# Performance work log

Hardware: AMD Instinct MI355X
Metric: run time of the kernel (lower is better)

Reference implementation:

```python
import jax, jax.numpy as jnp
import numpy as np

N, E, D, K = 32768, 16384, 4, 8          # nodes, hyperedges, edges/node, nodes/edge
IN_DIM, OUT_DIM, EDGE_DIM, NUM_HEADS = 128, 128, 64, 8


def setup_inputs() -> dict:
    key = jax.random.key(0)
    ks = jax.random.split(key, 16)
    s_in = 1.0 / np.sqrt(IN_DIM)
    s_out = 1.0 / np.sqrt(OUT_DIM)
    s_edge = 1.0 / np.sqrt(EDGE_DIM)
    return {
        "x": jax.random.normal(ks[0], (N, IN_DIM), jnp.float32),
        "edge_attr": jax.random.normal(ks[1], (E, EDGE_DIM), jnp.float32),
        "node_edges": jax.random.randint(ks[2], (N, D), 0, E),   # hyperedges containing each node
        "edge_nodes": jax.random.randint(ks[3], (E, K), 0, N),   # nodes inside each hyperedge
        "W_lin": jax.random.normal(ks[4], (OUT_DIM, IN_DIM), jnp.float32) * s_in,
        "W_edge": jax.random.normal(ks[5], (OUT_DIM, EDGE_DIM), jnp.float32) * s_edge,
        "Wq": jax.random.normal(ks[6], (OUT_DIM, OUT_DIM), jnp.float32) * s_out,
        "Wk": jax.random.normal(ks[7], (OUT_DIM, OUT_DIM), jnp.float32) * s_out,
        "Wv": jax.random.normal(ks[8], (OUT_DIM, OUT_DIM), jnp.float32) * s_out,
        "bq": jnp.zeros((OUT_DIM,), jnp.float32),
        "bk": jnp.zeros((OUT_DIM,), jnp.float32),
        "bv": jnp.zeros((OUT_DIM,), jnp.float32),
        "Wo": jax.random.normal(ks[9], (OUT_DIM, OUT_DIM), jnp.float32) * s_out,
        "bo": jnp.zeros((OUT_DIM,), jnp.float32),
    }


def reference(x, edge_attr, node_edges, edge_nodes,
              W_lin, W_edge, Wq, Wk, Wv, bq, bk, bv, Wo, bo):
    n, out_dim = x.shape[0], W_lin.shape[0]
    hd = out_dim // NUM_HEADS
    L = node_edges.shape[1] * edge_nodes.shape[1]  # D*K keys per node

    Wh = x @ W_lin.T                               # [N, out]
    We = edge_attr @ W_edge.T                      # [E, out]

    u_idx = edge_nodes[node_edges]                 # [N, D, K] neighbor node ids
    vals = Wh[u_idx]                               # [N, D, K, out]
    keys = vals + We[node_edges][:, :, None, :]    # key = Wh[u] + We[e]
    keys = keys.reshape(n, L, out_dim)
    vals = vals.reshape(n, L, out_dim)

    # torch nn.MultiheadAttention: single query per node (query = Wh[v])
    q = (Wh @ Wq.T + bq).reshape(n, NUM_HEADS, hd)
    k = (keys @ Wk.T + bk).reshape(n, L, NUM_HEADS, hd)
    v = (vals @ Wv.T + bv).reshape(n, L, NUM_HEADS, hd)

    scores = jnp.einsum('nhd,nlhd->nhl', q, k) / jnp.sqrt(jnp.asarray(hd, q.dtype))
    attn = jax.nn.softmax(scores, axis=-1)         # [N, H, L]
    ctx = jnp.einsum('nhl,nlhd->nhd', attn, v).reshape(n, out_dim)
    out = ctx @ Wo.T + bo
    return jax.nn.relu(out)
```

## Files before the change

kernel.cpp:

```cpp
#include <hip/hip_runtime.h>

#define N_NODES 32768
#define N_EDGES 16384
#define DEG 4
#define KPE 8
#define DIM 128
#define EDIM 64

typedef float f32x4 __attribute__((ext_vector_type(4)));
typedef __bf16 bf16x8 __attribute__((ext_vector_type(8)));
typedef __bf16 bf16x2 __attribute__((ext_vector_type(2)));
typedef unsigned short u16x8 __attribute__((ext_vector_type(8)));
typedef unsigned int u32;
typedef unsigned int u32x4 __attribute__((ext_vector_type(4)));
typedef int i32x4 __attribute__((ext_vector_type(4)));

static __device__ __forceinline__ unsigned short f2bf(float f) {
  union { float f; unsigned int u; } v; v.f = f;
  unsigned int r = (v.u + 0x7FFFu + ((v.u >> 16) & 1u)) >> 16;
  return (unsigned short)r;
}
static __device__ __forceinline__ float bflo(unsigned int v) {
  union { unsigned int u; float f; } x; x.u = v << 16; return x.f;
}
static __device__ __forceinline__ float bfhi(unsigned int v) {
  union { unsigned int u; float f; } x; x.u = v & 0xffff0000u; return x.f;
}

#if __has_builtin(__builtin_amdgcn_fdot2_f32_bf16)
static __device__ __forceinline__ float dot2bf(unsigned int a, unsigned int b, float c) {
  return __builtin_amdgcn_fdot2_f32_bf16(
      __builtin_bit_cast(bf16x2, a), __builtin_bit_cast(bf16x2, b), c, false);
}
#else
static __device__ __forceinline__ float dot2bf(unsigned int a, unsigned int b, float c) {
  c = fmaf(bflo(a), bflo(b), c);
  return fmaf(bfhi(a), bfhi(b), c);
}
#endif

__global__ __launch_bounds__(256) void wprep_kernel(
    const float* __restrict__ Wq, const float* __restrict__ Wk,
    const float* __restrict__ Wv, const float* __restrict__ Wlin,
    const float* __restrict__ Wedge, const float* __restrict__ Wo,
    const int* __restrict__ node_edges, const int* __restrict__ enodes,
    unsigned short* __restrict__ CW, unsigned short* __restrict__ CWE,
    unsigned short* __restrict__ Wob, int* __restrict__ uidx)
{
  int id = blockIdx.x * 256 + threadIdx.x;
  if (id < 384 * 128) {
    int j = id >> 7, i = id & 127;
    const float* wrow; float scale = 1.0f;
    if (j < 128)      { wrow = Wq + j * 128; scale = 0.25f; }
    else if (j < 256) { wrow = Wk + (j - 128) * 128; }
    else              { wrow = Wv + (j - 256) * 128; }
    float s = 0.f;
    #pragma unroll 8
    for (int m = 0; m < 128; ++m) s += wrow[m] * Wlin[m * 128 + i];
    CW[id] = f2bf(s * scale);
  } else if (id < 384 * 128 + 128 * 64) {
    int id2 = id - 384 * 128; int j = id2 >> 6, t = id2 & 63;
    float s = 0.f;
    #pragma unroll 8
    for (int m = 0; m < 128; ++m) s += Wk[j * 128 + m] * Wedge[m * 64 + t];
    CWE[id2] = f2bf(s);
  } else if (id < 384 * 128 + 128 * 64 + 128 * 128) {
    int id3 = id - (384 * 128 + 128 * 64);
    Wob[id3] = f2bf(Wo[id3]);
  } else {
    int t = id - (384 * 128 + 128 * 64 + 128 * 128);
    int e = node_edges[t];
    i32x4 a = *(const i32x4*)(enodes + (size_t)e * KPE);
    i32x4 b = *(const i32x4*)(enodes + (size_t)e * KPE + 4);
    *(i32x4*)(uidx + (size_t)t * KPE)     = a;
    *(i32x4*)(uidx + (size_t)t * KPE + 4) = b;
  }
}

__global__ __launch_bounds__(256) void g12_kernel(
    const float* __restrict__ x, const unsigned short* __restrict__ CW,
    const float* __restrict__ bq, const float* __restrict__ bv,
    unsigned short* __restrict__ qb, unsigned short* __restrict__ Kb,
    unsigned short* __restrict__ Vb,
    const float* __restrict__ ea, const unsigned short* __restrict__ CWE,
    const float* __restrict__ bk, unsigned short* __restrict__ WeKb)
{
  const int wave = threadIdx.x >> 6, lane = threadIdx.x & 63;
  const int r16 = lane & 15, quad = lane >> 4;

  if (blockIdx.x < 512) {
    const int m0 = blockIdx.x * 64 + wave * 16;
    u16x8 av[4];
    const float* arow = x + (size_t)(m0 + r16) * DIM + quad * 8;
    #pragma unroll
    for (int kk = 0; kk < 4; ++kk) {
      float4 a0 = *(const float4*)(arow + kk * 32);
      float4 a1 = *(const float4*)(arow + kk * 32 + 4);
      u16x8 au;
      au[0] = f2bf(a0.x); au[1] = f2bf(a0.y); au[2] = f2bf(a0.z); au[3] = f2bf(a0.w);
      au[4] = f2bf(a1.x); au[5] = f2bf(a1.y); au[6] = f2bf(a1.z); au[7] = f2bf(a1.w);
      av[kk] = au;
    }
    #pragma unroll
    for (int g = 0; g < 6; ++g) {
      f32x4 acc[4];
      const f32x4 z = {0.f, 0.f, 0.f, 0.f};
      acc[0] = z; acc[1] = z; acc[2] = z; acc[3] = z;
      #pragma unroll
      for (int kk = 0; kk < 4; ++kk) {
        #pragma unroll
        for (int s = 0; s < 4; ++s) {
          u16x8 bu = *(const u16x8*)(CW + (size_t)(g * 64 + s * 16 + r16) * DIM + kk * 32 + quad * 8);
          acc[s] = __builtin_amdgcn_mfma_f32_16x16x32_bf16(
              __builtin_bit_cast(bf16x8, av[kk]), __builtin_bit_cast(bf16x8, bu), acc[s], 0, 0, 0);
        }
      }
      const int arr = g >> 1;
      const int colbase = (g & 1) * 64;
      unsigned short* dst = arr == 0 ? qb : (arr == 1 ? Kb : Vb);
      #pragma unroll
      for (int s = 0; s < 4; ++s) {
        int j = colbase + s * 16 + r16;
        float bias = arr == 0 ? 0.25f * bq[j] : (arr == 2 ? bv[j] : 0.f);
        #pragma unroll
        for (int r = 0; r < 4; ++r) {
          int m = m0 + quad * 4 + r;
          dst[(size_t)m * DIM + j] = f2bf(acc[s][r] + bias);
        }
      }
    }
  } else {
    const int idx = blockIdx.x - 512;
    const int m0 = (idx >> 1) * 64 + wave * 16;
    const int n0 = (idx & 1) * 64;
    f32x4 acc[4];
    const f32x4 z = {0.f, 0.f, 0.f, 0.f};
    acc[0] = z; acc[1] = z; acc[2] = z; acc[3] = z;
    const float* arow = ea + (size_t)(m0 + r16) * EDIM + quad * 8;
    #pragma unroll
    for (int kk = 0; kk < 2; ++kk) {
      float4 a0 = *(const float4*)(arow + kk * 32);
      float4 a1 = *(const float4*)(arow + kk * 32 + 4);
      u16x8 au;
      au[0] = f2bf(a0.x); au[1] = f2bf(a0.y); au[2] = f2bf(a0.z); au[3] = f2bf(a0.w);
      au[4] = f2bf(a1.x); au[5] = f2bf(a1.y); au[6] = f2bf(a1.z); au[7] = f2bf(a1.w);
      bf16x8 av = __builtin_bit_cast(bf16x8, au);
      #pragma unroll
      for (int s = 0; s < 4; ++s) {
        u16x8 bu = *(const u16x8*)(CWE + (size_t)(n0 + s * 16 + r16) * EDIM + kk * 32 + quad * 8);
        acc[s] = __builtin_amdgcn_mfma_f32_16x16x32_bf16(
            av, __builtin_bit_cast(bf16x8, bu), acc[s], 0, 0, 0);
      }
    }
    #pragma unroll
    for (int s = 0; s < 4; ++s) {
      int j = n0 + s * 16 + r16;
      float bias = bk[j];
      #pragma unroll
      for (int r = 0; r < 4; ++r) {
        int m = m0 + quad * 4 + r;
        WeKb[(size_t)m * DIM + j] = f2bf(acc[s][r] + bias);
      }
    }
  }
}

__global__ __launch_bounds__(256) void g2b_kernel(
    const unsigned short* __restrict__ Kb, const unsigned short* __restrict__ WeKb,
    const int* __restrict__ enodes, unsigned short* __restrict__ Ke)
{
  const int wave = threadIdx.x >> 6, lane = threadIdx.x & 63;
  const int e = blockIdx.x * 4 + wave;

  const int* ep = enodes + (size_t)e * KPE;
  i32x4 a = *(const i32x4*)ep;
  i32x4 b = *(const i32x4*)(ep + 4);
  u32 we = ((const u32*)(WeKb + (size_t)e * DIM))[lane];

  int id[8] = {a.x, a.y, a.z, a.w, b.x, b.y, b.z, b.w};
  u32 kr[8];
  #pragma unroll
  for (int t = 0; t < 8; ++t)
    kr[t] = ((const u32*)(Kb + (size_t)id[t] * DIM))[lane];

  const float wl = bflo(we), wh = bfhi(we);
  u32* out = (u32*)(Ke + (size_t)e * KPE * DIM);
  #pragma unroll
  for (int t = 0; t < 8; ++t) {
    u32 pk = (u32)f2bf(bflo(kr[t]) + wl) | ((u32)f2bf(bfhi(kr[t]) + wh) << 16);
    out[t * (DIM / 2) + lane] = pk;
  }
}

__global__ __launch_bounds__(64, 3) void attn_kernel(
    const unsigned short* __restrict__ qb, const unsigned short* __restrict__ Ke,
    const unsigned short* __restrict__ Vb,
    const int* __restrict__ nedges, const int* __restrict__ uidx,
    unsigned short* __restrict__ ctxb)
{
  __shared__ __align__(16) float ldsP[8][36];
  const int lane = threadIdx.x;
  const int n = blockIdx.x;
  const int l = lane & 31, half = lane >> 5;
  const int h = lane >> 3;
  const int c0 = lane * 2;

  i32x4 e4 = __builtin_nontemporal_load((const i32x4*)(nedges + (size_t)n * DEG));
  const i32x4* up = (const i32x4*)(uidx + (size_t)n * 32);
  i32x4 m0 = __builtin_nontemporal_load(up + 0);
  i32x4 m1 = __builtin_nontemporal_load(up + 1);
  i32x4 m2 = __builtin_nontemporal_load(up + 2);
  i32x4 m3 = __builtin_nontemporal_load(up + 3);
  i32x4 m4 = __builtin_nontemporal_load(up + 4);
  i32x4 m5 = __builtin_nontemporal_load(up + 5);
  i32x4 m6 = __builtin_nontemporal_load(up + 6);
  i32x4 m7 = __builtin_nontemporal_load(up + 7);

  const u32x4* qp = (const u32x4*)(qb + (size_t)n * DIM + half * 64);
  u32x4 qv[8];
  #pragma unroll
  for (int ch = 0; ch < 8; ++ch) qv[ch] = __builtin_nontemporal_load(qp + ch);

  asm volatile("" ::: "memory");

  const int d = l >> 3, kk = l & 7;
  int el = d == 0 ? e4.x : (d == 1 ? e4.y : (d == 2 ? e4.z : e4.w));
  const unsigned short* krow = Ke + ((size_t)el * KPE + kk) * DIM + half * 64;
  u32x4 kc[8];
  #pragma unroll
  for (int ch = 0; ch < 8; ++ch) kc[ch] = *(const u32x4*)(krow + ch * 8);

  asm volatile("" ::: "memory");

  u32 vv[32];
#define VLOAD(t, row) vv[t] = *(const u32*)(Vb + (size_t)(row) * DIM + c0)
  VLOAD(0,  m0.x); VLOAD(1,  m0.y); VLOAD(2,  m0.z); VLOAD(3,  m0.w);
  VLOAD(4,  m1.x); VLOAD(5,  m1.y); VLOAD(6,  m1.z); VLOAD(7,  m1.w);
  VLOAD(8,  m2.x); VLOAD(9,  m2.y); VLOAD(10, m2.z); VLOAD(11, m2.w);
  VLOAD(12, m3.x); VLOAD(13, m3.y); VLOAD(14, m3.z); VLOAD(15, m3.w);
  VLOAD(16, m4.x); VLOAD(17, m4.y); VLOAD(18, m4.z); VLOAD(19, m4.w);
  VLOAD(20, m5.x); VLOAD(21, m5.y); VLOAD(22, m5.z); VLOAD(23, m5.w);
  VLOAD(24, m6.x); VLOAD(25, m6.y); VLOAD(26, m6.z); VLOAD(27, m6.w);
  VLOAD(28, m7.x); VLOAD(29, m7.y); VLOAD(30, m7.z); VLOAD(31, m7.w);
#undef VLOAD

  asm volatile("" ::: "memory");

  float s[4] = {0.f, 0.f, 0.f, 0.f};
  #pragma unroll
  for (int ch = 0; ch < 8; ++ch) {
    const int hi = ch >> 1;
    float t = s[hi];
    t = dot2bf(qv[ch].x, kc[ch].x, t);
    t = dot2bf(qv[ch].y, kc[ch].y, t);
    t = dot2bf(qv[ch].z, kc[ch].z, t);
    t = dot2bf(qv[ch].w, kc[ch].w, t);
    s[hi] = t;
  }

  #pragma unroll
  for (int hi = 0; hi < 4; ++hi) {
    float vmax = s[hi];
    #pragma unroll
    for (int off = 16; off >= 1; off >>= 1)
      vmax = fmaxf(vmax, __shfl_xor(vmax, off, 32));
    float ex = __expf(s[hi] - vmax);
    float sum = ex;
    #pragma unroll
    for (int off = 16; off >= 1; off >>= 1)
      sum += __shfl_xor(sum, off, 32);
    ldsP[half * 4 + hi][l] = ex / sum;
  }

  float a0 = 0.f, a1 = 0.f;
  #pragma unroll
  for (int t = 0; t < 8; ++t) {
    float4 p4 = *(const float4*)&ldsP[h][t * 4];
    a0 = fmaf(p4.x, bflo(vv[t * 4 + 0]), a0); a1 = fmaf(p4.x, bfhi(vv[t * 4 + 0]), a1);
    a0 = fmaf(p4.y, bflo(vv[t * 4 + 1]), a0); a1 = fmaf(p4.y, bfhi(vv[t * 4 + 1]), a1);
    a0 = fmaf(p4.z, bflo(vv[t * 4 + 2]), a0); a1 = fmaf(p4.z, bfhi(vv[t * 4 + 2]), a1);
    a0 = fmaf(p4.w, bflo(vv[t * 4 + 3]), a0); a1 = fmaf(p4.w, bfhi(vv[t * 4 + 3]), a1);
  }
  unsigned int pk = (unsigned int)f2bf(a0) | ((unsigned int)f2bf(a1) << 16);
  __builtin_nontemporal_store(pk, (u32*)(ctxb + (size_t)n * DIM + c0));
}

__global__ __launch_bounds__(256) void g4_kernel(
    const unsigned short* __restrict__ ctxb, const unsigned short* __restrict__ Wob,
    const float* __restrict__ bo, float* __restrict__ out)
{
  const int wave = threadIdx.x >> 6, lane = threadIdx.x & 63;
  const int r16 = lane & 15, quad = lane >> 4;
  const int m0 = blockIdx.x * 64 + wave * 16;
  const int n0 = blockIdx.y * 64;

  f32x4 acc[4];
  const f32x4 z = {0.f, 0.f, 0.f, 0.f};
  acc[0] = z; acc[1] = z; acc[2] = z; acc[3] = z;

  #pragma unroll
  for (int kk = 0; kk < 4; ++kk) {
    u16x8 au = *(const u16x8*)(ctxb + (size_t)(m0 + r16) * DIM + kk * 32 + quad * 8);
    bf16x8 av = __builtin_bit_cast(bf16x8, au);
    #pragma unroll
    for (int s = 0; s < 4; ++s) {
      u16x8 bu = *(const u16x8*)(Wob + (size_t)(n0 + s * 16 + r16) * DIM + kk * 32 + quad * 8);
      acc[s] = __builtin_amdgcn_mfma_f32_16x16x32_bf16(
          av, __builtin_bit_cast(bf16x8, bu), acc[s], 0, 0, 0);
    }
  }

  #pragma unroll
  for (int s = 0; s < 4; ++s) {
    int j = n0 + s * 16 + r16;
    float bias = bo[j];
    #pragma unroll
    for (int r = 0; r < 4; ++r) {
      int m = m0 + quad * 4 + r;
      float v = acc[s][r] + bias;
      out[(size_t)m * DIM + j] = v > 0.f ? v : 0.f;
    }
  }
}

extern "C" void kernel_launch(void* const* d_in, const int* in_sizes, int n_in,
                              void* d_out, int out_size, void* d_ws, size_t ws_size,
                              hipStream_t stream)
{
  const float* x     = (const float*)d_in[0];
  const float* ea    = (const float*)d_in[1];
  const int* nedges  = (const int*)d_in[2];
  const int* enodes  = (const int*)d_in[3];
  const float* Wlin  = (const float*)d_in[4];
  const float* Wedge = (const float*)d_in[5];
  const float* Wq    = (const float*)d_in[6];
  const float* Wk    = (const float*)d_in[7];
  const float* Wv    = (const float*)d_in[8];
  const float* bq    = (const float*)d_in[9];
  const float* bk    = (const float*)d_in[10];
  const float* bv    = (const float*)d_in[11];
  const float* Wo    = (const float*)d_in[12];
  const float* bo    = (const float*)d_in[13];
  float* out = (float*)d_out;

  unsigned short* wsp = (unsigned short*)d_ws;
  unsigned short* CW   = wsp;  wsp += 384 * 128;
  unsigned short* CWE  = wsp;  wsp += 128 * 64;
  unsigned short* Wob  = wsp;  wsp += 128 * 128;
  unsigned short* qb   = wsp;  wsp += (size_t)N_NODES * DIM;
  unsigned short* Kb   = wsp;  wsp += (size_t)N_NODES * DIM;
  unsigned short* Vb   = wsp;  wsp += (size_t)N_NODES * DIM;
  unsigned short* WeKb = wsp;  wsp += (size_t)N_EDGES * DIM;
  unsigned short* ctxb = wsp;  wsp += (size_t)N_NODES * DIM;
  int* uidx = (int*)wsp;       wsp += (size_t)N_NODES * 32 * 2;
  unsigned short* Ke   = wsp;  wsp += (size_t)N_EDGES * KPE * DIM;

  wprep_kernel<<<dim3(800), dim3(256), 0, stream>>>(
      Wq, Wk, Wv, Wlin, Wedge, Wo, nedges, enodes, CW, CWE, Wob, uidx);
  g12_kernel<<<dim3(1024), dim3(256), 0, stream>>>(x, CW, bq, bv, qb, Kb, Vb, ea, CWE, bk, WeKb);
  g2b_kernel<<<dim3(N_EDGES / 4), dim3(256), 0, stream>>>(Kb, WeKb, enodes, Ke);
  attn_kernel<<<dim3(32768), dim3(64), 0, stream>>>(qb, Ke, Vb, nedges, uidx, ctxb);
  g4_kernel<<<dim3(512, 2), dim3(256), 0, stream>>>(ctxb, Wob, bo, out);
}
```

Before: 219.6 us.

## Restructure attention edge-centric with reverse index and per-edge score and context kernels

```diff
diff --git a/kernel.cpp b/kernel.cpp
--- a/kernel.cpp
+++ b/kernel.cpp
@@ -6,6 +6,7 @@
 #define KPE 8
 #define DIM 128
 #define EDIM 64
+#define MAXC 64
 
 typedef float f32x4 __attribute__((ext_vector_type(4)));
 typedef __bf16 bf16x8 __attribute__((ext_vector_type(8)));
@@ -26,6 +27,12 @@
 static __device__ __forceinline__ float bfhi(unsigned int v) {
   union { unsigned int u; float f; } x; x.u = v & 0xffff0000u; return x.f;
 }
+static __device__ __forceinline__ float f16tof(unsigned short h) {
+  return (float)__builtin_bit_cast(_Float16, h);
+}
+static __device__ __forceinline__ unsigned short ftof16(float f) {
+  return __builtin_bit_cast(unsigned short, (_Float16)f);
+}
 
 #if __has_builtin(__builtin_amdgcn_fdot2_f32_bf16)
 static __device__ __forceinline__ float dot2bf(unsigned int a, unsigned int b, float c) {
@@ -39,13 +46,18 @@
 }
 #endif
 
+__global__ __launch_bounds__(256) void zcnt_kernel(int* __restrict__ cnt)
+{
+  cnt[blockIdx.x * 256 + threadIdx.x] = 0;
+}
+
 __global__ __launch_bounds__(256) void wprep_kernel(
     const float* __restrict__ Wq, const float* __restrict__ Wk,
     const float* __restrict__ Wv, const float* __restrict__ Wlin,
     const float* __restrict__ Wedge, const float* __restrict__ Wo,
-    const int* __restrict__ node_edges, const int* __restrict__ enodes,
+    const int* __restrict__ node_edges,
     unsigned short* __restrict__ CW, unsigned short* __restrict__ CWE,
-    unsigned short* __restrict__ Wob, int* __restrict__ uidx)
+    unsigned short* __restrict__ Wob, int* __restrict__ cnt, int* __restrict__ rev)
 {
   int id = blockIdx.x * 256 + threadIdx.x;
   if (id < 384 * 128) {
@@ -69,11 +81,11 @@
     Wob[id3] = f2bf(Wo[id3]);
   } else {
     int t = id - (384 * 128 + 128 * 64 + 128 * 128);
-    int e = node_edges[t];
-    i32x4 a = *(const i32x4*)(enodes + (size_t)e * KPE);
-    i32x4 b = *(const i32x4*)(enodes + (size_t)e * KPE + 4);
-    *(i32x4*)(uidx + (size_t)t * KPE)     = a;
-    *(i32x4*)(uidx + (size_t)t * KPE + 4) = b;
+    if (t < N_NODES * DEG) {
+      int e = node_edges[t];
+      int pos = atomicAdd(&cnt[e], 1);
+      if (pos < MAXC) rev[(size_t)e * MAXC + pos] = t;
+    }
   }
 }
 
@@ -165,160 +177,178 @@
   }
 }
 
-__global__ __launch_bounds__(256) void g2b_kernel(
-    const unsigned short* __restrict__ Kb, const unsigned short* __restrict__ WeKb,
-    const int* __restrict__ enodes, unsigned short* __restrict__ Ke)
+__global__ __launch_bounds__(256) void escore_kernel(
+    const unsigned short* __restrict__ qb, const unsigned short* __restrict__ Kb,
+    const unsigned short* __restrict__ WeKb, const int* __restrict__ enodes,
+    const int* __restrict__ cnt, const int* __restrict__ rev,
+    unsigned short* __restrict__ S)
 {
   const int wave = threadIdx.x >> 6, lane = threadIdx.x & 63;
   const int e = blockIdx.x * 4 + wave;
-
-  const int* ep = enodes + (size_t)e * KPE;
-  i32x4 a = *(const i32x4*)ep;
-  i32x4 b = *(const i32x4*)(ep + 4);
-  u32 we = ((const u32*)(WeKb + (size_t)e * DIM))[lane];
-
-  int id[8] = {a.x, a.y, a.z, a.w, b.x, b.y, b.z, b.w};
-  u32 kr[8];
-  #pragma unroll
-  for (int t = 0; t < 8; ++t)
-    kr[t] = ((const u32*)(Kb + (size_t)id[t] * DIM))[lane];
-
-  const float wl = bflo(we), wh = bfhi(we);
-  u32* out = (u32*)(Ke + (size_t)e * KPE * DIM);
-  #pragma unroll
-  for (int t = 0; t < 8; ++t) {
-    u32 pk = (u32)f2bf(bflo(kr[t]) + wl) | ((u32)f2bf(bfhi(kr[t]) + wh) << 16);
-    out[t * (DIM / 2) + lane] = pk;
-  }
-}
-
-__global__ __launch_bounds__(64, 3) void attn_kernel(
-    const unsigned short* __restrict__ qb, const unsigned short* __restrict__ Ke,
-    const unsigned short* __restrict__ Vb,
-    const int* __restrict__ nedges, const int* __restrict__ uidx,
-    unsigned short* __restrict__ ctxb)
-{
-  __shared__ __align__(16) float ldsP[8][36];
-  const int lane = threadIdx.x;
-  const int n = blockIdx.x;
-  const int l = lane & 31, half = lane >> 5;
-  const int h = lane >> 3;
-  const int c0 = lane * 2;
-
-  i32x4 e4 = __builtin_nontemporal_load((const i32x4*)(nedges + (size_t)n * DEG));
-  const i32x4* up = (const i32x4*)(uidx + (size_t)n * 32);
-  i32x4 m0 = __builtin_nontemporal_load(up + 0);
-  i32x4 m1 = __builtin_nontemporal_load(up + 1);
-  i32x4 m2 = __builtin_nontemporal_load(up + 2);
-  i32x4 m3 = __builtin_nontemporal_load(up + 3);
-  i32x4 m4 = __builtin_nontemporal_load(up + 4);
-  i32x4 m5 = __builtin_nontemporal_load(up + 5);
-  i32x4 m6 = __builtin_nontemporal_load(up + 6);
-  i32x4 m7 = __builtin_nontemporal_load(up + 7);
-
-  const u32x4* qp = (const u32x4*)(qb + (size_t)n * DIM + half * 64);
-  u32x4 qv[8];
-  #pragma unroll
-  for (int ch = 0; ch < 8; ++ch) qv[ch] = __builtin_nontemporal_load(qp + ch);
-
-  asm volatile("" ::: "memory");
-
-  const int d = l >> 3, kk = l & 7;
-  int el = d == 0 ? e4.x : (d == 1 ? e4.y : (d == 2 ? e4.z : e4.w));
-  const unsigned short* krow = Ke + ((size_t)el * KPE + kk) * DIM + half * 64;
-  u32x4 kc[8];
-  #pragma unroll
-  for (int ch = 0; ch < 8; ++ch) kc[ch] = *(const u32x4*)(krow + ch * 8);
-
-  asm volatile("" ::: "memory");
-
-  u32 vv[32];
-#define VLOAD(t, row) vv[t] = *(const u32*)(Vb + (size_t)(row) * DIM + c0)
-  VLOAD(0,  m0.x); VLOAD(1,  m0.y); VLOAD(2,  m0.z); VLOAD(3,  m0.w);
-  VLOAD(4,  m1.x); VLOAD(5,  m1.y); VLOAD(6,  m1.z); VLOAD(7,  m1.w);
-  VLOAD(8,  m2.x); VLOAD(9,  m2.y); VLOAD(10, m2.z); VLOAD(11, m2.w);
-  VLOAD(12, m3.x); VLOAD(13, m3.y); VLOAD(14, m3.z); VLOAD(15, m3.w);
-  VLOAD(16, m4.x); VLOAD(17, m4.y); VLOAD(18, m4.z); VLOAD(19, m4.w);
-  VLOAD(20, m5.x); VLOAD(21, m5.y); VLOAD(22, m5.z); VLOAD(23, m5.w);
-  VLOAD(24, m6.x); VLOAD(25, m6.y); VLOAD(26, m6.z); VLOAD(27, m6.w);
-  VLOAD(28, m7.x); VLOAD(29, m7.y); VLOAD(30, m7.z); VLOAD(31, m7.w);
-#undef VLOAD
-
-  asm volatile("" ::: "memory");
-
-  float s[4] = {0.f, 0.f, 0.f, 0.f};
-  #pragma unroll
-  for (int ch = 0; ch < 8; ++ch) {
-    const int hi = ch >> 1;
-    float t = s[hi];
-    t = dot2bf(qv[ch].x, kc[ch].x, t);
-    t = dot2bf(qv[ch].y, kc[ch].y, t);
-    t = dot2bf(qv[ch].z, kc[ch].z, t);
-    t = dot2bf(qv[ch].w, kc[ch].w, t);
-    s[hi] = t;
-  }
-
+  const int g = lane >> 3, j = lane & 7;
+
+  int c_n = cnt[e]; if (c_n > MAXC) c_n = MAXC;
+  if (c_n == 0) return;
+  int rv = rev[(size_t)e * MAXC + lane];
+
+  int mid = enodes[(size_t)e * KPE + g];
+  u32x4 k0 = *(const u32x4*)(Kb + (size_t)mid * DIM + j * 16);
+  u32x4 k1 = *(const u32x4*)(Kb + (size_t)mid * DIM + j * 16 + 8);
+  u32x4 w0 = *(const u32x4*)(WeKb + (size_t)e * DIM + j * 16);
+  u32x4 w1 = *(const u32x4*)(WeKb + (size_t)e * DIM + j * 16 + 8);
+
+  int pk = __shfl(rv, 0);
+  u32x4 qa0 = *(const u32x4*)(qb + (size_t)(pk >> 2) * DIM + j * 16);
+  u32x4 qa1 = *(const u32x4*)(qb + (size_t)(pk >> 2) * DIM + j * 16 + 8);
+
+  for (int c = 0; c < c_n; ++c) {
+    const int n = pk >> 2, d = pk & 3;
+    u32x4 q0 = qa0, q1 = qa1;
+    if (c + 1 < c_n) {
+      pk = __shfl(rv, c + 1);
+      qa0 = *(const u32x4*)(qb + (size_t)(pk >> 2) * DIM + j * 16);
+      qa1 = *(const u32x4*)(qb + (size_t)(pk >> 2) * DIM + j * 16 + 8);
+    }
+    float s = 0.f;
+    s = dot2bf(q0.x, k0.x, s); s = dot2bf(q0.y, k0.y, s);
+    s = dot2bf(q0.z, k0.z, s); s = dot2bf(q0.w, k0.w, s);
+    s = dot2bf(q1.x, k1.x, s); s = dot2bf(q1.y, k1.y, s);
+    s = dot2bf(q1.z, k1.z, s); s = dot2bf(q1.w, k1.w, s);
+    s = dot2bf(q0.x, w0.x, s); s = dot2bf(q0.y, w0.y, s);
+    s = dot2bf(q0.z, w0.z, s); s = dot2bf(q0.w, w0.w, s);
+    s = dot2bf(q1.x, w1.x, s); s = dot2bf(q1.y, w1.y, s);
+    s = dot2bf(q1.z, w1.z, s); s = dot2bf(q1.w, w1.w, s);
+    S[(size_t)n * 256 + d * 64 + g * 8 + j] = ftof16(s);
+  }
+}
+
+__global__ __launch_bounds__(256) void nsm_kernel(unsigned short* __restrict__ SP)
+{
+  const int wave = threadIdx.x >> 6, lane = threadIdx.x & 63;
+  const int n = blockIdx.x * 4 + wave;
+  const int l = lane & 31, hp = lane >> 5;
+  unsigned short* row = SP + (size_t)n * 256;
+
+  uint2 sv = *(const uint2*)(row + l * 8 + hp * 4);
+  float s4[4] = { f16tof(sv.x & 0xffff), f16tof(sv.x >> 16),
+                  f16tof(sv.y & 0xffff), f16tof(sv.y >> 16) };
+  unsigned short pr[4];
   #pragma unroll
   for (int hi = 0; hi < 4; ++hi) {
-    float vmax = s[hi];
+    float vmax = s4[hi];
     #pragma unroll
     for (int off = 16; off >= 1; off >>= 1)
       vmax = fmaxf(vmax, __shfl_xor(vmax, off, 32));
-    float ex = __expf(s[hi] - vmax);
+    float ex = __expf(s4[hi] - vmax);
     float sum = ex;
     #pragma unroll
     for (int off = 16; off >= 1; off >>= 1)
       sum += __shfl_xor(sum, off, 32);
-    ldsP[half * 4 + hi][l] = ex / sum;
-  }
-
-  float a0 = 0.f, a1 = 0.f;
-  #pragma unroll
-  for (int t = 0; t < 8; ++t) {
-    float4 p4 = *(const float4*)&ldsP[h][t * 4];
-    a0 = fmaf(p4.x, bflo(vv[t * 4 + 0]), a0); a1 = fmaf(p4.x, bfhi(vv[t * 4 + 0]), a1);
-    a0 = fmaf(p4.y, bflo(vv[t * 4 + 1]), a0); a1 = fmaf(p4.y, bfhi(vv[t * 4 + 1]), a1);
-    a0 = fmaf(p4.z, bflo(vv[t * 4 + 2]), a0); a1 = fmaf(p4.z, bfhi(vv[t * 4 + 2]), a1);
-    a0 = fmaf(p4.w, bflo(vv[t * 4 + 3]), a0); a1 = fmaf(p4.w, bfhi(vv[t * 4 + 3]), a1);
-  }
-  unsigned int pk = (unsigned int)f2bf(a0) | ((unsigned int)f2bf(a1) << 16);
-  __builtin_nontemporal_store(pk, (u32*)(ctxb + (size_t)n * DIM + c0));
+    pr[hi] = ftof16(ex / sum);
+  }
+  #pragma unroll
+  for (int hi = 0; hi < 4; ++hi)
+    row[(hp * 4 + hi) * 32 + l] = pr[hi];
+}
+
+__global__ __launch_bounds__(256) void ectx_kernel(
+    const unsigned short* __restrict__ Vb, const unsigned short* __restrict__ P,
+    const int* __restrict__ enodes, const int* __restrict__ cnt,
+    const int* __restrict__ rev, unsigned short* __restrict__ ctxp)
+{
+  const int wave = threadIdx.x >> 6, lane = threadIdx.x & 63;
+  const int e = blockIdx.x * 4 + wave;
+  const int c0 = lane * 2, h = lane >> 3;
+
+  int c_n = cnt[e]; if (c_n > MAXC) c_n = MAXC;
+  if (c_n == 0) return;
+  int rv = rev[(size_t)e * MAXC + lane];
+
+  const int* ep = enodes + (size_t)e * KPE;
+  i32x4 a4 = *(const i32x4*)ep;
+  i32x4 b4 = *(const i32x4*)(ep + 4);
+  int id[8] = {a4.x, a4.y, a4.z, a4.w, b4.x, b4.y, b4.z, b4.w};
+  u32 vv[8];
+  #pragma unroll
+  for (int k = 0; k < 8; ++k) vv[k] = *(const u32*)(Vb + (size_t)id[k] * DIM + c0);
+
+  int pk = __shfl(rv, 0);
+  uint4 pva = *(const uint4*)(P + (size_t)(pk >> 2) * 256 + h * 32 + (pk & 3) * 8);
+
+  for (int c = 0; c < c_n; ++c) {
+    const int n = pk >> 2, d = pk & 3;
+    uint4 pv = pva;
+    if (c + 1 < c_n) {
+      pk = __shfl(rv, c + 1);
+      pva = *(const uint4*)(P + (size_t)(pk >> 2) * 256 + h * 32 + (pk & 3) * 8);
+    }
+    float p0 = f16tof(pv.x & 0xffff), p1 = f16tof(pv.x >> 16);
+    float p2 = f16tof(pv.y & 0xffff), p3 = f16tof(pv.y >> 16);
+    float p4 = f16tof(pv.z & 0xffff), p5 = f16tof(pv.z >> 16);
+    float p6 = f16tof(pv.w & 0xffff), p7 = f16tof(pv.w >> 16);
+    float a0 = 0.f, a1 = 0.f;
+    a0 = fmaf(p0, bflo(vv[0]), a0); a1 = fmaf(p0, bfhi(vv[0]), a1);
+    a0 = fmaf(p1, bflo(vv[1]), a0); a1 = fmaf(p1, bfhi(vv[1]), a1);
+    a0 = fmaf(p2, bflo(vv[2]), a0); a1 = fmaf(p2, bfhi(vv[2]), a1);
+    a0 = fmaf(p3, bflo(vv[3]), a0); a1 = fmaf(p3, bfhi(vv[3]), a1);
+    a0 = fmaf(p4, bflo(vv[4]), a0); a1 = fmaf(p4, bfhi(vv[4]), a1);
+    a0 = fmaf(p5, bflo(vv[5]), a0); a1 = fmaf(p5, bfhi(vv[5]), a1);
+    a0 = fmaf(p6, bflo(vv[6]), a0); a1 = fmaf(p6, bfhi(vv[6]), a1);
+    a0 = fmaf(p7, bflo(vv[7]), a0); a1 = fmaf(p7, bfhi(vv[7]), a1);
+    u32 pk2 = (u32)ftof16(a0) | ((u32)ftof16(a1) << 16);
+    *(u32*)(ctxp + ((size_t)n * 4 + d) * DIM + c0) = pk2;
+  }
 }
 
 __global__ __launch_bounds__(256) void g4_kernel(
-    const unsigned short* __restrict__ ctxb, const unsigned short* __restrict__ Wob,
+    const unsigned short* __restrict__ ctxp, const unsigned short* __restrict__ Wob,
     const float* __restrict__ bo, float* __restrict__ out)
 {
   const int wave = threadIdx.x >> 6, lane = threadIdx.x & 63;
   const int r16 = lane & 15, quad = lane >> 4;
   const int m0 = blockIdx.x * 64 + wave * 16;
-  const int n0 = blockIdx.y * 64;
-
-  f32x4 acc[4];
+
+  f32x4 acc[2][4];
   const f32x4 z = {0.f, 0.f, 0.f, 0.f};
-  acc[0] = z; acc[1] = z; acc[2] = z; acc[3] = z;
+  #pragma unroll
+  for (int hf = 0; hf < 2; ++hf) { acc[hf][0] = z; acc[hf][1] = z; acc[hf][2] = z; acc[hf][3] = z; }
 
   #pragma unroll
   for (int kk = 0; kk < 4; ++kk) {
-    u16x8 au = *(const u16x8*)(ctxb + (size_t)(m0 + r16) * DIM + kk * 32 + quad * 8);
+    float fa[8] = {0.f, 0.f, 0.f, 0.f, 0.f, 0.f, 0.f, 0.f};
+    #pragma unroll
+    for (int d = 0; d < 4; ++d) {
+      u16x8 t = *(const u16x8*)(ctxp + ((size_t)(m0 + r16) * 4 + d) * DIM + kk * 32 + quad * 8);
+      #pragma unroll
+      for (int i = 0; i < 8; ++i) fa[i] += f16tof(t[i]);
+    }
+    u16x8 au;
+    #pragma unroll
+    for (int i = 0; i < 8; ++i) au[i] = f2bf(fa[i]);
     bf16x8 av = __builtin_bit_cast(bf16x8, au);
     #pragma unroll
+    for (int hf = 0; hf < 2; ++hf) {
+      #pragma unroll
+      for (int s = 0; s < 4; ++s) {
+        u16x8 bu = *(const u16x8*)(Wob + (size_t)(hf * 64 + s * 16 + r16) * DIM + kk * 32 + quad * 8);
+        acc[hf][s] = __builtin_amdgcn_mfma_f32_16x16x32_bf16(
+            av, __builtin_bit_cast(bf16x8, bu), acc[hf][s], 0, 0, 0);
+      }
+    }
+  }
+
+  #pragma unroll
+  for (int hf = 0; hf < 2; ++hf) {
+    #pragma unroll
     for (int s = 0; s < 4; ++s) {
-      u16x8 bu = *(const u16x8*)(Wob + (size_t)(n0 + s * 16 + r16) * DIM + kk * 32 + quad * 8);
-      acc[s] = __builtin_amdgcn_mfma_f32_16x16x32_bf16(
-          av, __builtin_bit_cast(bf16x8, bu), acc[s], 0, 0, 0);
-    }
-  }
-
-  #pragma unroll
-  for (int s = 0; s < 4; ++s) {
-    int j = n0 + s * 16 + r16;
-    float bias = bo[j];
-    #pragma unroll
-    for (int r = 0; r < 4; ++r) {
-      int m = m0 + quad * 4 + r;
-      float v = acc[s][r] + bias;
-      out[(size_t)m * DIM + j] = v > 0.f ? v : 0.f;
+      int jj = hf * 64 + s * 16 + r16;
+      float bias = bo[jj];
+      #pragma unroll
+      for (int r = 0; r < 4; ++r) {
+        int m = m0 + quad * 4 + r;
+        float v = acc[hf][s][r] + bias;
+        out[(size_t)m * DIM + jj] = v > 0.f ? v : 0.f;
+      }
     }
   }
 }
@@ -351,14 +381,17 @@
   unsigned short* Kb   = wsp;  wsp += (size_t)N_NODES * DIM;
   unsigned short* Vb   = wsp;  wsp += (size_t)N_NODES * DIM;
   unsigned short* WeKb = wsp;  wsp += (size_t)N_EDGES * DIM;
-  unsigned short* ctxb = wsp;  wsp += (size_t)N_NODES * DIM;
-  int* uidx = (int*)wsp;       wsp += (size_t)N_NODES * 32 * 2;
-  unsigned short* Ke   = wsp;  wsp += (size_t)N_EDGES * KPE * DIM;
-
+  unsigned short* SP   = wsp;  wsp += (size_t)N_NODES * 256;
+  unsigned short* ctxp = wsp;  wsp += (size_t)N_NODES * 4 * DIM;
+  int* cnt = (int*)wsp;        wsp += N_EDGES * 2;
+  int* rev = (int*)wsp;        wsp += (size_t)N_EDGES * MAXC * 2;
+
+  zcnt_kernel<<<dim3(64), dim3(256), 0, stream>>>(cnt);
   wprep_kernel<<<dim3(800), dim3(256), 0, stream>>>(
-      Wq, Wk, Wv, Wlin, Wedge, Wo, nedges, enodes, CW, CWE, Wob, uidx);
+      Wq, Wk, Wv, Wlin, Wedge, Wo, nedges, CW, CWE, Wob, cnt, rev);
   g12_kernel<<<dim3(1024), dim3(256), 0, stream>>>(x, CW, bq, bv, qb, Kb, Vb, ea, CWE, bk, WeKb);
-  g2b_kernel<<<dim3(N_EDGES / 4), dim3(256), 0, stream>>>(Kb, WeKb, enodes, Ke);
-  attn_kernel<<<dim3(32768), dim3(64), 0, stream>>>(qb, Ke, Vb, nedges, uidx, ctxb);
-  g4_kernel<<<dim3(512, 2), dim3(256), 0, stream>>>(ctxb, Wob, bo, out);
-}
+  escore_kernel<<<dim3(N_EDGES / 4), dim3(256), 0, stream>>>(qb, Kb, WeKb, enodes, cnt, rev, SP);
+  nsm_kernel<<<dim3(N_NODES / 4), dim3(256), 0, stream>>>(SP);
+  ectx_kernel<<<dim3(N_EDGES / 4), dim3(256), 0, stream>>>(Vb, SP, enodes, cnt, rev, ctxp);
+  g4_kernel<<<dim3(512), dim3(256), 0, stream>>>(ctxp, Wob, bo, out);
+}
```

Measured after the change: 207.5 us. 1.06x faster.
